# Kernel tuning notes

Hardware: AMD Instinct MI355X
Metric: run time of the kernel (lower is better)

## Reference

```python
import jax, jax.numpy as jnp
import numpy as np

B, N = 8, 2048
IN_F, MID1, HID, MID2, OUT_F = 128, 128, 128, 128, 128
BIG = 9e15  # matches torch's 9000000000000000.0 additive mask constant


def _linear_params(key, out_d, in_d):
    # torch Linear layout: W is [out, in]
    kw, kb = jax.random.split(key)
    w = jax.random.normal(kw, (out_d, in_d), jnp.float32) * (1.0 / np.sqrt(in_d))
    b = jax.random.normal(kb, (out_d,), jnp.float32) * 0.01
    return w, b


def setup_inputs() -> dict:
    key = jax.random.key(0)
    ks = jax.random.split(key, 16)
    h = jax.random.normal(ks[0], (B, N, IN_F), jnp.float32)
    adj = jax.random.randint(ks[1], (B, N, N), 0, 2).astype(jnp.float32)
    vae2_fetures = jax.random.normal(ks[2], (B, N, OUT_F), jnp.float32)
    Wv1, bv1 = _linear_params(ks[3], MID1, IN_F)
    Wk1, bk1 = _linear_params(ks[4], MID1, IN_F)
    Wq1, bq1 = _linear_params(ks[5], MID1, IN_F)
    Wo1, bo1 = _linear_params(ks[6], HID, MID1)
    Wv2, bv2 = _linear_params(ks[7], MID2, HID)
    Wk2, bk2 = _linear_params(ks[8], MID2, HID)
    Wq2, bq2 = _linear_params(ks[9], MID2, HID)
    Wo2, bo2 = _linear_params(ks[10], OUT_F, MID2)
    Wf, bf = _linear_params(ks[11], OUT_F, 2 * OUT_F)
    return {
        "h": h, "adj": adj, "vae2_fetures": vae2_fetures,
        "Wv1": Wv1, "bv1": bv1, "Wk1": Wk1, "bk1": bk1, "Wq1": Wq1, "bq1": bq1,
        "Wo1": Wo1, "bo1": bo1,
        "Wv2": Wv2, "bv2": bv2, "Wk2": Wk2, "bk2": bk2, "Wq2": Wq2, "bq2": bq2,
        "Wo2": Wo2, "bo2": bo2, "Wf": Wf, "bf": bf,
    }


def _lin(x, W, b):
    return jnp.einsum('bnd,od->bno', x, W) + b


def _masked_att_block(x, adj, Wq, bq, Wk, bk, Wv, bv):
    v = jax.nn.relu(_lin(x, Wv, bv))          # [B,N,D]
    q = jax.nn.relu(_lin(x, Wq, bq))          # [B,N,D]
    k = jax.nn.relu(_lin(x, Wk, bk))          # [B,N,D]
    s = jnp.einsum('bnd,bmd->bnm', q, k)       # [B,N,N]
    masked = s * adj - BIG * (1.0 - adj)       # multiplicative + additive mask
    att = jax.nn.softmax(masked, axis=-1)
    return jnp.einsum('bnm,bmd->bnd', att, v)


def reference(h, adj, vae2_fetures,
              Wv1, bv1, Wk1, bk1, Wq1, bq1, Wo1, bo1,
              Wv2, bv2, Wk2, bk2, Wq2, bq2, Wo2, bo2,
              Wf, bf):
    f1 = _masked_att_block(h, adj, Wq1, bq1, Wk1, bk1, Wv1, bv1)
    f1 = _lin(f1, Wo1, bo1)                    # [B,N,HID]
    f2 = _masked_att_block(f1, adj, Wq2, bq2, Wk2, bk2, Wv2, bv2)
    f2 = _lin(f2, Wo2, bo2)                    # [B,N,OUT_F]
    f3 = jnp.concatenate([f2, vae2_fetures], axis=2)
    return _lin(f3, Wf, bf)                    # [B,N,OUT_F]
```

## Files before the change

kernel.cpp:

```cpp
#include <hip/hip_runtime.h>

typedef short s16x8 __attribute__((ext_vector_type(8)));
typedef float f32x4 __attribute__((ext_vector_type(4)));
typedef unsigned short u16x4v __attribute__((ext_vector_type(4)));

#define NSPLIT 4
#define NROWS 16384
#define MSHIFT 44.0f

__device__ __forceinline__ unsigned short f2bf(float f) {
  union { float fl; unsigned int i; } v; v.fl = f;
  unsigned int x = v.i;
  x += 0x7fffu + ((x >> 16) & 1u);
  return (unsigned short)(x >> 16);
}
__device__ __forceinline__ s16x8 load8_bf16(const unsigned short* p) {
  return *(const s16x8*)p;
}
__device__ __forceinline__ s16x8 load8_f32(const float* p) {
  float4 a = *(const float4*)p;
  float4 b = *(const float4*)(p + 4);
  s16x8 r;
  r[0] = (short)f2bf(a.x); r[1] = (short)f2bf(a.y);
  r[2] = (short)f2bf(a.z); r[3] = (short)f2bf(a.w);
  r[4] = (short)f2bf(b.x); r[5] = (short)f2bf(b.y);
  r[6] = (short)f2bf(b.z); r[7] = (short)f2bf(b.w);
  return r;
}
__device__ __forceinline__ int vperm(int nn) {
  return (nn & ~31) | (((nn >> 2) & 3) << 3) | (((nn >> 4) & 1) << 2);
}

__device__ __forceinline__ void gload16(const void* g, void* l) {
  __builtin_amdgcn_global_load_lds(
      (const __attribute__((address_space(1))) void*)g,
      (__attribute__((address_space(3))) void*)l, 16, 0, 0);
}

__device__ __forceinline__ void pack_adj_body(
    const float* __restrict__ ADJ, unsigned long long* __restrict__ MASK,
    int pblk)
{
  const int t = threadIdx.x;
  const int w = t >> 6;
  const int lane = t & 63;
  const int row0 = pblk * 32 + w * 8;

  for (int i = 0; i < 8; ++i) {
    const int row = row0 + i;
    const float4* src = (const float4*)(ADJ + (size_t)row * 2048);
    float4 v[8];
#pragma unroll
    for (int j = 0; j < 8; ++j) v[j] = src[j * 64 + lane];

    unsigned long long wm = 0ull;
#pragma unroll
    for (int j = 0; j < 8; ++j) {
      const unsigned long long b0 = __ballot(v[j].x != 0.f);
      wm = (lane == j * 4 + 0) ? b0 : wm;
      const unsigned long long b1 = __ballot(v[j].y != 0.f);
      wm = (lane == j * 4 + 1) ? b1 : wm;
      const unsigned long long b2 = __ballot(v[j].z != 0.f);
      wm = (lane == j * 4 + 2) ? b2 : wm;
      const unsigned long long b3 = __ballot(v[j].w != 0.f);
      wm = (lane == j * 4 + 3) ? b3 : wm;
    }
    if (lane < 32) MASK[(size_t)row * 32 + lane] = wm;
  }
}

__device__ __forceinline__ void qkv_merged_body(
    const float* __restrict__ X,
    const float* __restrict__ Wq, const float* __restrict__ bq, unsigned short* __restrict__ oq,
    const float* __restrict__ Wk, const float* __restrict__ bk, unsigned short* __restrict__ ok,
    const float* __restrict__ Wv, const float* __restrict__ bv, unsigned short* __restrict__ ovt)
{
  const int t = threadIdx.x;
  const int w = t >> 6;
  const int lane = t & 63;
  const int l15 = lane & 15;
  const int quad = lane >> 4;
  const int mbase = blockIdx.x * 64;

  s16x8 af[4][4];
#pragma unroll
  for (int mt = 0; mt < 4; ++mt) {
    const float* ar = X + (size_t)(mbase + mt * 16 + l15) * 128;
#pragma unroll
    for (int ks = 0; ks < 4; ++ks) af[mt][ks] = load8_f32(ar + ks * 32 + quad * 8);
  }

  const float* Ws[3] = {Wq, Wk, Wv};
  const float* bs[3] = {bq, bk, bv};
  unsigned short* outs[3] = {oq, ok, ovt};

#pragma unroll
  for (int which = 0; which < 3; ++which) {
    const float* W = Ws[which];
    const float* bias = bs[which];
    unsigned short* out = outs[which];
#pragma unroll
    for (int nt = 0; nt < 2; ++nt) {
      const int n = (w * 2 + nt) * 16 + l15;
      const float* wr = W + (size_t)n * 128;
      s16x8 wf[4];
#pragma unroll
      for (int ks = 0; ks < 4; ++ks) wf[ks] = load8_f32(wr + ks * 32 + quad * 8);
      f32x4 acc[4];
#pragma unroll
      for (int mt = 0; mt < 4; ++mt) acc[mt] = (f32x4){0.f, 0.f, 0.f, 0.f};
#pragma unroll
      for (int mt = 0; mt < 4; ++mt)
#pragma unroll
        for (int ks = 0; ks < 4; ++ks)
          acc[mt] = __builtin_amdgcn_mfma_f32_16x16x32_bf16(af[mt][ks], wf[ks], acc[mt], 0, 0, 0);
      const float bv_ = bias[n];
      if (which < 2) {
#pragma unroll
        for (int mt = 0; mt < 4; ++mt)
#pragma unroll
          for (int r = 0; r < 4; ++r)
            out[(size_t)(mbase + mt * 16 + quad * 4 + r) * 128 + n] =
                f2bf(fmaxf(acc[mt][r] + bv_, 0.f));
      } else {
        const int b = mbase >> 11;
#pragma unroll
        for (int mt = 0; mt < 4; ++mt) {
          const int nn = (mbase & 2047) + mt * 16 + quad * 4;
          u16x4v pk;
#pragma unroll
          for (int r = 0; r < 4; ++r) pk[r] = f2bf(fmaxf(acc[mt][r] + bv_, 0.f));
          *(u16x4v*)(out + (size_t)(b * 128 + n) * 2048 + vperm(nn)) = pk;
        }
      }
    }
  }
}

__global__ __launch_bounds__(256) void qkv1_kernel(
    const float* __restrict__ x,
    const float* __restrict__ Wq, const float* __restrict__ bq, unsigned short* __restrict__ oq,
    const float* __restrict__ Wk, const float* __restrict__ bk, unsigned short* __restrict__ ok,
    const float* __restrict__ Wv, const float* __restrict__ bv, unsigned short* __restrict__ ovt,
    const float* __restrict__ adj, unsigned long long* __restrict__ mask)
{
  if (blockIdx.x < 256) qkv_merged_body(x, Wq, bq, oq, Wk, bk, ok, Wv, bv, ovt);
  else                  pack_adj_body(adj, mask, blockIdx.x - 256);
}

__global__ __launch_bounds__(256, 2) void attn_kernel(
    const unsigned short* __restrict__ Q,
    const unsigned short* __restrict__ K,
    const unsigned short* __restrict__ VT,
    const unsigned long long* __restrict__ MASK,
    float* __restrict__ pO, float* __restrict__ pl)
{
  __shared__ __align__(16) unsigned short kbuf[2][64][128];
  __shared__ __align__(16) unsigned short vbuf[2][128][64];

  const int t = threadIdx.x;
  const int w = t >> 6;
  const int lane = t & 63;
  const int l15 = lane & 15;
  const int quad = lane >> 4;
  const int x7 = l15 & 7;

  const int gq0 = blockIdx.x * 128;
  const int b   = gq0 >> 11;
  const int wq0 = (gq0 & 2047) + w * 32;
  const int kc0 = blockIdx.y * (2048 / NSPLIT);

  const unsigned short* Kb  = K  + (size_t)(b * 2048) * 128;
  const unsigned short* VTb = VT + (size_t)(b * 128) * 2048;
  const unsigned long long* Mb = MASK + (size_t)b * 2048 * 32;

  const int krow = t >> 4;
  const int kc16 = t & 15;
  const int kchunk = kc16 ^ (krow & 7);
  const int vrow = t >> 3;
  const int vc16 = t & 7;
  const int vchunk = vc16 ^ (vrow & 7);

  s16x8 qf[2][4];
#pragma unroll
  for (int mt = 0; mt < 2; ++mt) {
    const unsigned short* qrow = Q + (size_t)(gq0 + w * 32 + mt * 16 + l15) * 128;
#pragma unroll
    for (int ks = 0; ks < 4; ++ks) qf[mt][ks] = load8_bf16(qrow + ks * 32 + quad * 8);
  }

  s16x8 ones;
#pragma unroll
  for (int i = 0; i < 8; ++i) ones[i] = (short)0x3F80;

  f32x4 accO[2][8];
  f32x4 accL[2];
#pragma unroll
  for (int mt = 0; mt < 2; ++mt) {
    accL[mt] = (f32x4){0.f, 0.f, 0.f, 0.f};
#pragma unroll
    for (int dt = 0; dt < 8; ++dt) accO[mt][dt] = (f32x4){0.f, 0.f, 0.f, 0.f};
  }

#pragma unroll
  for (int i = 0; i < 4; ++i)
    gload16(Kb + (size_t)(kc0 + i * 16 + krow) * 128 + kchunk * 8,
            &kbuf[0][i * 16 + krow][kc16 * 8]);
#pragma unroll
  for (int i = 0; i < 4; ++i)
    gload16(VTb + (size_t)(i * 32 + vrow) * 2048 + kc0 + vchunk * 8,
            &vbuf[0][i * 32 + vrow][vc16 * 8]);

  __syncthreads();

  for (int g = 0; g < 2; ++g) {
    const int jj = (kc0 >> 8) + g;
    ulonglong2 m01[2], m23[2];
#pragma unroll
    for (int mt = 0; mt < 2; ++mt) {
      const unsigned long long* mrow = Mb + (size_t)(wq0 + mt * 16 + l15) * 32 + jj * 4;
      m01[mt] = *(const ulonglong2*)mrow;
      m23[mt] = *(const ulonglong2*)(mrow + 2);
    }

#pragma unroll
    for (int cg = 0; cg < 4; ++cg) {
      const int kc = kc0 + g * 256 + cg * 64;
      unsigned short (*kb)[128] = kbuf[cg & 1];
      unsigned short (*vb)[64]  = vbuf[cg & 1];

      if (g == 0 || cg < 3) {
        unsigned short (*kbn)[128] = kbuf[(cg + 1) & 1];
        unsigned short (*vbn)[64]  = vbuf[(cg + 1) & 1];
#pragma unroll
        for (int i = 0; i < 4; ++i)
          gload16(Kb + (size_t)(kc + 64 + i * 16 + krow) * 128 + kchunk * 8,
                  &kbn[i * 16 + krow][kc16 * 8]);
#pragma unroll
        for (int i = 0; i < 4; ++i)
          gload16(VTb + (size_t)(i * 32 + vrow) * 2048 + (kc + 64) + vchunk * 8,
                  &vbn[i * 32 + vrow][vc16 * 8]);
      }

      f32x4 sv[2][4];
#pragma unroll
      for (int nt = 0; nt < 4; ++nt) {
        sv[0][nt] = (f32x4){0.f, 0.f, 0.f, 0.f};
        sv[1][nt] = (f32x4){0.f, 0.f, 0.f, 0.f};
      }
      __builtin_amdgcn_s_setprio(1);
#pragma unroll
      for (int nt = 0; nt < 4; ++nt)
#pragma unroll
        for (int ks = 0; ks < 4; ++ks) {
          s16x8 kf = *(const s16x8*)&kb[nt * 16 + l15][((ks * 4 + quad) ^ x7) * 8];
          sv[0][nt] = __builtin_amdgcn_mfma_f32_16x16x32_bf16(kf, qf[0][ks], sv[0][nt], 0, 0, 0);
          sv[1][nt] = __builtin_amdgcn_mfma_f32_16x16x32_bf16(kf, qf[1][ks], sv[1][nt], 0, 0, 0);
        }
      __builtin_amdgcn_s_setprio(0);

      s16x8 pf[2][2];
#pragma unroll
      for (int mt = 0; mt < 2; ++mt) {
        const unsigned long long bse0 = m01[mt].x >> (cg * 16 + quad);
        const unsigned long long bse1 = m01[mt].y >> (cg * 16 + quad);
        const unsigned long long bse2 = m23[mt].x >> (cg * 16 + quad);
        const unsigned long long bse3 = m23[mt].y >> (cg * 16 + quad);
#pragma unroll
        for (int ks = 0; ks < 2; ++ks) {
          s16x8 v;
#pragma unroll
          for (int half = 0; half < 2; ++half) {
            const int nt = ks * 2 + half;
#pragma unroll
            for (int r = 0; r < 4; ++r) {
              const float e = __expf(sv[mt][nt][r] - MSHIFT);
              const unsigned long long bw = (r == 0) ? bse0 : (r == 1) ? bse1
                                          : (r == 2) ? bse2 : bse3;
              const bool keep = (bw >> (nt * 4)) & 1ull;
              v[half * 4 + r] = (short)f2bf(keep ? e : 0.f);
            }
          }
          pf[mt][ks] = v;
        }
      }

      __builtin_amdgcn_s_setprio(1);
#pragma unroll
      for (int mt = 0; mt < 2; ++mt)
#pragma unroll
        for (int ks = 0; ks < 2; ++ks)
          accL[mt] = __builtin_amdgcn_mfma_f32_16x16x32_bf16(ones, pf[mt][ks], accL[mt], 0, 0, 0);

#pragma unroll
      for (int dt = 0; dt < 8; ++dt)
#pragma unroll
        for (int ks = 0; ks < 2; ++ks) {
          s16x8 vf = *(const s16x8*)&vb[dt * 16 + l15][((ks * 4 + quad) ^ x7) * 8];
          accO[0][dt] = __builtin_amdgcn_mfma_f32_16x16x32_bf16(vf, pf[0][ks], accO[0][dt], 0, 0, 0);
          accO[1][dt] = __builtin_amdgcn_mfma_f32_16x16x32_bf16(vf, pf[1][ks], accO[1][dt], 0, 0, 0);
        }
      __builtin_amdgcn_s_setprio(0);

      __syncthreads();
    }
  }

  float* pOs = pO + (size_t)blockIdx.y * NROWS * 128;
#pragma unroll
  for (int mt = 0; mt < 2; ++mt) {
    const int qg = gq0 + w * 32 + mt * 16 + l15;
#pragma unroll
    for (int dt = 0; dt < 8; ++dt)
      *(f32x4*)(pOs + (size_t)qg * 128 + dt * 16 + quad * 4) = accO[mt][dt];
  }
  if (quad == 0) {
#pragma unroll
    for (int mt = 0; mt < 2; ++mt)
      pl[blockIdx.y * NROWS + gq0 + w * 32 + mt * 16 + l15] = accL[mt][0];
  }
}

__device__ __forceinline__ void combine64(
    const float* __restrict__ pO, const float* __restrict__ pl, int grow0,
    unsigned short (*At)[136])
{
  const int t = threadIdx.x;
#pragma unroll
  for (int u = 0; u < 4; ++u) {
    const int unit = u * 256 + t;
    const int row = unit >> 4;
    const int col8 = (unit & 15) * 8;
    const int grow = grow0 + row;
    float lsum = 0.f;
#pragma unroll
    for (int s = 0; s < NSPLIT; ++s) lsum += pl[s * NROWS + grow];
    const float inv = (lsum > 0.f) ? 1.f / lsum : 0.f;
    float acc8[8];
#pragma unroll
    for (int i = 0; i < 8; ++i) acc8[i] = 0.f;
#pragma unroll
    for (int s = 0; s < NSPLIT; ++s) {
      const float* p = pO + (size_t)s * NROWS * 128 + (size_t)grow * 128 + col8;
      float4 x0 = *(const float4*)p;
      float4 x1 = *(const float4*)(p + 4);
      acc8[0] += x0.x; acc8[1] += x0.y; acc8[2] += x0.z; acc8[3] += x0.w;
      acc8[4] += x1.x; acc8[5] += x1.y; acc8[6] += x1.z; acc8[7] += x1.w;
    }
#pragma unroll
    for (int i = 0; i < 8; ++i) At[row][col8 + i] = f2bf(acc8[i] * inv);
  }
}

__global__ __launch_bounds__(256) void redqkv_kernel(
    const float* __restrict__ pO, const float* __restrict__ pl,
    const float* __restrict__ Wo, const float* __restrict__ bo,
    const float* __restrict__ Wq, const float* __restrict__ bq, unsigned short* __restrict__ oq,
    const float* __restrict__ Wk, const float* __restrict__ bk, unsigned short* __restrict__ ok,
    const float* __restrict__ Wv, const float* __restrict__ bv, unsigned short* __restrict__ ovt)
{
  __shared__ __align__(16) unsigned short At[64][136];
  __shared__ __align__(16) unsigned short Bt[64][136];
  const int t = threadIdx.x;
  const int grow0 = blockIdx.x * 64;

  combine64(pO, pl, grow0, At);
  __syncthreads();

  const int w = t >> 6;
  const int lane = t & 63;
  const int l15 = lane & 15;
  const int quad = lane >> 4;

  s16x8 af[4][4];
#pragma unroll
  for (int mt = 0; mt < 4; ++mt)
#pragma unroll
    for (int ks = 0; ks < 4; ++ks)
      af[mt][ks] = *(const s16x8*)&At[mt * 16 + l15][ks * 32 + quad * 8];

#pragma unroll
  for (int nt = 0; nt < 2; ++nt) {
    const int n = (w * 2 + nt) * 16 + l15;
    const float* wr = Wo + (size_t)n * 128;
    s16x8 wf[4];
#pragma unroll
    for (int ks = 0; ks < 4; ++ks) wf[ks] = load8_f32(wr + ks * 32 + quad * 8);
    f32x4 acc[4];
#pragma unroll
    for (int mt = 0; mt < 4; ++mt) acc[mt] = (f32x4){0.f, 0.f, 0.f, 0.f};
#pragma unroll
    for (int mt = 0; mt < 4; ++mt)
#pragma unroll
      for (int ks = 0; ks < 4; ++ks)
        acc[mt] = __builtin_amdgcn_mfma_f32_16x16x32_bf16(af[mt][ks], wf[ks], acc[mt], 0, 0, 0);
    const float bv_ = bo[n];
#pragma unroll
    for (int mt = 0; mt < 4; ++mt)
#pragma unroll
      for (int r = 0; r < 4; ++r)
        Bt[mt * 16 + quad * 4 + r][n] = f2bf(acc[mt][r] + bv_);
  }
  __syncthreads();

  s16x8 a2[4][4];
#pragma unroll
  for (int mt = 0; mt < 4; ++mt)
#pragma unroll
    for (int ks = 0; ks < 4; ++ks)
      a2[mt][ks] = *(const s16x8*)&Bt[mt * 16 + l15][ks * 32 + quad * 8];

#pragma unroll
  for (int which = 0; which < 3; ++which) {
    const float* W = (which == 0) ? Wq : (which == 1) ? Wk : Wv;
    const float* bb = (which == 0) ? bq : (which == 1) ? bk : bv;
    unsigned short* out = (which == 0) ? oq : (which == 1) ? ok : ovt;
#pragma unroll
    for (int nt = 0; nt < 2; ++nt) {
      const int n = (w * 2 + nt) * 16 + l15;
      const float* wr = W + (size_t)n * 128;
      s16x8 wf[4];
#pragma unroll
      for (int ks = 0; ks < 4; ++ks) wf[ks] = load8_f32(wr + ks * 32 + quad * 8);
      f32x4 acc[4];
#pragma unroll
      for (int mt = 0; mt < 4; ++mt) acc[mt] = (f32x4){0.f, 0.f, 0.f, 0.f};
#pragma unroll
      for (int mt = 0; mt < 4; ++mt)
#pragma unroll
        for (int ks = 0; ks < 4; ++ks)
          acc[mt] = __builtin_amdgcn_mfma_f32_16x16x32_bf16(a2[mt][ks], wf[ks], acc[mt], 0, 0, 0);
      const float bv_ = bb[n];
      if (which < 2) {
#pragma unroll
        for (int mt = 0; mt < 4; ++mt)
#pragma unroll
          for (int r = 0; r < 4; ++r)
            out[(size_t)(grow0 + mt * 16 + quad * 4 + r) * 128 + n] =
                f2bf(fmaxf(acc[mt][r] + bv_, 0.f));
      } else {
        const int b = grow0 >> 11;
#pragma unroll
        for (int mt = 0; mt < 4; ++mt) {
          const int nn = (grow0 & 2047) + mt * 16 + quad * 4;
          u16x4v pk;
#pragma unroll
          for (int r = 0; r < 4; ++r) pk[r] = f2bf(fmaxf(acc[mt][r] + bv_, 0.f));
          *(u16x4v*)(out + (size_t)(b * 128 + n) * 2048 + vperm(nn)) = pk;
        }
      }
    }
  }
}

__global__ __launch_bounds__(256) void redfinal_kernel(
    const float* __restrict__ pO, const float* __restrict__ pl,
    const float* __restrict__ Wo, const float* __restrict__ bo,
    const float* __restrict__ Wf, const float* __restrict__ bff,
    const float* __restrict__ vae2, float* __restrict__ out)
{
  __shared__ __align__(16) unsigned short At[64][136];
  __shared__ __align__(16) unsigned short Bt[64][136];
  const int t = threadIdx.x;
  const int grow0 = blockIdx.x * 64;

  combine64(pO, pl, grow0, At);
  __syncthreads();

  const int w = t >> 6;
  const int lane = t & 63;
  const int l15 = lane & 15;
  const int quad = lane >> 4;

  s16x8 af[4][4];
#pragma unroll
  for (int mt = 0; mt < 4; ++mt)
#pragma unroll
    for (int ks = 0; ks < 4; ++ks)
      af[mt][ks] = *(const s16x8*)&At[mt * 16 + l15][ks * 32 + quad * 8];

#pragma unroll
  for (int nt = 0; nt < 2; ++nt) {
    const int n = (w * 2 + nt) * 16 + l15;
    const float* wr = Wo + (size_t)n * 128;
    s16x8 wf[4];
#pragma unroll
    for (int ks = 0; ks < 4; ++ks) wf[ks] = load8_f32(wr + ks * 32 + quad * 8);
    f32x4 acc[4];
#pragma unroll
    for (int mt = 0; mt < 4; ++mt) acc[mt] = (f32x4){0.f, 0.f, 0.f, 0.f};
#pragma unroll
    for (int mt = 0; mt < 4; ++mt)
#pragma unroll
      for (int ks = 0; ks < 4; ++ks)
        acc[mt] = __builtin_amdgcn_mfma_f32_16x16x32_bf16(af[mt][ks], wf[ks], acc[mt], 0, 0, 0);
    const float bv_ = bo[n];
#pragma unroll
    for (int mt = 0; mt < 4; ++mt)
#pragma unroll
      for (int r = 0; r < 4; ++r)
        Bt[mt * 16 + quad * 4 + r][n] = f2bf(acc[mt][r] + bv_);
  }
  __syncthreads();

  s16x8 a1[4][4], a2[4][4];
#pragma unroll
  for (int mt = 0; mt < 4; ++mt) {
#pragma unroll
    for (int ks = 0; ks < 4; ++ks)
      a1[mt][ks] = *(const s16x8*)&Bt[mt * 16 + l15][ks * 32 + quad * 8];
    const float* vrow = vae2 + (size_t)(grow0 + mt * 16 + l15) * 128;
#pragma unroll
    for (int ks = 0; ks < 4; ++ks) a2[mt][ks] = load8_f32(vrow + ks * 32 + quad * 8);
  }

#pragma unroll
  for (int nt = 0; nt < 2; ++nt) {
    const int n = (w * 2 + nt) * 16 + l15;
    const float* wr = Wf + (size_t)n * 256;
    s16x8 wfl[4], wfr[4];
#pragma unroll
    for (int ks = 0; ks < 4; ++ks) {
      wfl[ks] = load8_f32(wr + ks * 32 + quad * 8);
      wfr[ks] = load8_f32(wr + 128 + ks * 32 + quad * 8);
    }
    f32x4 acc[4];
#pragma unroll
    for (int mt = 0; mt < 4; ++mt) acc[mt] = (f32x4){0.f, 0.f, 0.f, 0.f};
#pragma unroll
    for (int mt = 0; mt < 4; ++mt) {
#pragma unroll
      for (int ks = 0; ks < 4; ++ks)
        acc[mt] = __builtin_amdgcn_mfma_f32_16x16x32_bf16(a1[mt][ks], wfl[ks], acc[mt], 0, 0, 0);
#pragma unroll
      for (int ks = 0; ks < 4; ++ks)
        acc[mt] = __builtin_amdgcn_mfma_f32_16x16x32_bf16(a2[mt][ks], wfr[ks], acc[mt], 0, 0, 0);
    }
    const float bv_ = bff[n];
#pragma unroll
    for (int mt = 0; mt < 4; ++mt)
#pragma unroll
      for (int r = 0; r < 4; ++r)
        out[(size_t)(grow0 + mt * 16 + quad * 4 + r) * 128 + n] = acc[mt][r] + bv_;
  }
}

extern "C" void kernel_launch(void* const* d_in, const int* in_sizes, int n_in,
                              void* d_out, int out_size, void* d_ws, size_t ws_size,
                              hipStream_t stream)
{
  const float* h    = (const float*)d_in[0];
  const float* adj  = (const float*)d_in[1];
  const float* vae2 = (const float*)d_in[2];
  const float* Wv1  = (const float*)d_in[3];
  const float* bv1  = (const float*)d_in[4];
  const float* Wk1  = (const float*)d_in[5];
  const float* bk1  = (const float*)d_in[6];
  const float* Wq1  = (const float*)d_in[7];
  const float* bq1  = (const float*)d_in[8];
  const float* Wo1  = (const float*)d_in[9];
  const float* bo1  = (const float*)d_in[10];
  const float* Wv2  = (const float*)d_in[11];
  const float* bv2  = (const float*)d_in[12];
  const float* Wk2  = (const float*)d_in[13];
  const float* bk2  = (const float*)d_in[14];
  const float* Wq2  = (const float*)d_in[15];
  const float* bq2  = (const float*)d_in[16];
  const float* Wo2  = (const float*)d_in[17];
  const float* bo2  = (const float*)d_in[18];
  const float* Wf   = (const float*)d_in[19];
  const float* bff  = (const float*)d_in[20];

  char* wsb = (char*)d_ws;
  const size_t MB = 1u << 20;
  unsigned short* s_q  = (unsigned short*)(wsb + 0 * MB);
  unsigned short* s_k  = (unsigned short*)(wsb + 4 * MB);
  unsigned short* s_vt = (unsigned short*)(wsb + 8 * MB);
  unsigned long long* maskp = (unsigned long long*)(wsb + 12 * MB);
  float* pO = (float*)(wsb + 16 * MB);
  float* pl = (float*)(wsb + 48 * MB);

  qkv1_kernel<<<dim3(256 + 512), dim3(256), 0, stream>>>(
      h, Wq1, bq1, s_q, Wk1, bk1, s_k, Wv1, bv1, s_vt, adj, maskp);
  attn_kernel<<<dim3(128, NSPLIT), dim3(256), 0, stream>>>(
      s_q, s_k, s_vt, maskp, pO, pl);
  redqkv_kernel<<<dim3(256), dim3(256), 0, stream>>>(
      pO, pl, Wo1, bo1, Wq2, bq2, s_q, Wk2, bk2, s_k, Wv2, bv2, s_vt);
  attn_kernel<<<dim3(128, NSPLIT), dim3(256), 0, stream>>>(
      s_q, s_k, s_vt, maskp, pO, pl);
  redfinal_kernel<<<dim3(256), dim3(256), 0, stream>>>(
      pO, pl, Wo2, bo2, Wf, bff, vae2, (float*)d_out);
}
```

Measured before the change: 357.2 us.

## Repack adjacency mask per-lane without ballots and split pack into separate kernel

Adjacency packing now has each lane read 32 contiguous floats and build a 32-bit word directly, instead of using 32 wavefront ballots per row. The bit layout is arranged so the attention kernel can take each lane's keep bits from one 32-bit word with simple shifts, rather than from four shifted 64-bit words. The fused qkv+pack launch is split into two separate kernels, which adds one launch and removes the concurrency between the GEMM and the pack. Per-lane contiguous 128-byte loads may coalesce less well than the previous strided float4 pattern.

```diff
diff --git a/kernel.cpp b/kernel.cpp
--- a/kernel.cpp
+++ b/kernel.cpp
@@ -37,39 +37,34 @@
       (__attribute__((address_space(3))) void*)l, 16, 0, 0);
 }
 
-__device__ __forceinline__ void pack_adj_body(
-    const float* __restrict__ ADJ, unsigned long long* __restrict__ MASK,
-    int pblk)
+__global__ __launch_bounds__(256) void pack_kernel(
+    const float* __restrict__ ADJ, unsigned int* __restrict__ MASK32)
 {
   const int t = threadIdx.x;
   const int w = t >> 6;
   const int lane = t & 63;
-  const int row0 = pblk * 32 + w * 8;
+  const int row0 = blockIdx.x * 32 + w * 8;
 
   for (int i = 0; i < 8; ++i) {
     const int row = row0 + i;
-    const float4* src = (const float4*)(ADJ + (size_t)row * 2048);
+    const float4* src = (const float4*)(ADJ + (size_t)row * 2048 + lane * 32);
     float4 v[8];
 #pragma unroll
-    for (int j = 0; j < 8; ++j) v[j] = src[j * 64 + lane];
-
-    unsigned long long wm = 0ull;
+    for (int j = 0; j < 8; ++j) v[j] = src[j];
+
+    unsigned int wm = 0u;
 #pragma unroll
     for (int j = 0; j < 8; ++j) {
-      const unsigned long long b0 = __ballot(v[j].x != 0.f);
-      wm = (lane == j * 4 + 0) ? b0 : wm;
-      const unsigned long long b1 = __ballot(v[j].y != 0.f);
-      wm = (lane == j * 4 + 1) ? b1 : wm;
-      const unsigned long long b2 = __ballot(v[j].z != 0.f);
-      wm = (lane == j * 4 + 2) ? b2 : wm;
-      const unsigned long long b3 = __ballot(v[j].w != 0.f);
-      wm = (lane == j * 4 + 3) ? b3 : wm;
-    }
-    if (lane < 32) MASK[(size_t)row * 32 + lane] = wm;
-  }
-}
-
-__device__ __forceinline__ void qkv_merged_body(
+      wm |= (v[j].x != 0.f ? 1u : 0u) << (4 * j);
+      wm |= (v[j].y != 0.f ? 2u : 0u) << (4 * j);
+      wm |= (v[j].z != 0.f ? 4u : 0u) << (4 * j);
+      wm |= (v[j].w != 0.f ? 8u : 0u) << (4 * j);
+    }
+    MASK32[(size_t)row * 64 + lane] = wm;
+  }
+}
+
+__global__ __launch_bounds__(256) void gemm_kernel(
     const float* __restrict__ X,
     const float* __restrict__ Wq, const float* __restrict__ bq, unsigned short* __restrict__ oq,
     const float* __restrict__ Wk, const float* __restrict__ bk, unsigned short* __restrict__ ok,
@@ -137,22 +132,11 @@
   }
 }
 
-__global__ __launch_bounds__(256) void qkv1_kernel(
-    const float* __restrict__ x,
-    const float* __restrict__ Wq, const float* __restrict__ bq, unsigned short* __restrict__ oq,
-    const float* __restrict__ Wk, const float* __restrict__ bk, unsigned short* __restrict__ ok,
-    const float* __restrict__ Wv, const float* __restrict__ bv, unsigned short* __restrict__ ovt,
-    const float* __restrict__ adj, unsigned long long* __restrict__ mask)
-{
-  if (blockIdx.x < 256) qkv_merged_body(x, Wq, bq, oq, Wk, bk, ok, Wv, bv, ovt);
-  else                  pack_adj_body(adj, mask, blockIdx.x - 256);
-}
-
 __global__ __launch_bounds__(256, 2) void attn_kernel(
     const unsigned short* __restrict__ Q,
     const unsigned short* __restrict__ K,
     const unsigned short* __restrict__ VT,
-    const unsigned long long* __restrict__ MASK,
+    const unsigned int* __restrict__ MASK32,
     float* __restrict__ pO, float* __restrict__ pl)
 {
   __shared__ __align__(16) unsigned short kbuf[2][64][128];
@@ -172,7 +156,7 @@
 
   const unsigned short* Kb  = K  + (size_t)(b * 2048) * 128;
   const unsigned short* VTb = VT + (size_t)(b * 128) * 2048;
-  const unsigned long long* Mb = MASK + (size_t)b * 2048 * 32;
+  const unsigned int* Mb32 = MASK32 + (size_t)b * 2048 * 64;
 
   const int krow = t >> 4;
   const int kc16 = t & 15;
@@ -215,12 +199,13 @@
 
   for (int g = 0; g < 2; ++g) {
     const int jj = (kc0 >> 8) + g;
-    ulonglong2 m01[2], m23[2];
+    uint4 ua[2], ub[2];
 #pragma unroll
     for (int mt = 0; mt < 2; ++mt) {
-      const unsigned long long* mrow = Mb + (size_t)(wq0 + mt * 16 + l15) * 32 + jj * 4;
-      m01[mt] = *(const ulonglong2*)mrow;
-      m23[mt] = *(const ulonglong2*)(mrow + 2);
+      const unsigned int* mrow =
+          Mb32 + (size_t)(wq0 + mt * 16 + l15) * 64 + jj * 8;
+      ua[mt] = *(const uint4*)mrow;
+      ub[mt] = *(const uint4*)(mrow + 4);
     }
 
 #pragma unroll
@@ -262,12 +247,15 @@
       s16x8 pf[2][2];
 #pragma unroll
       for (int mt = 0; mt < 2; ++mt) {
-        const unsigned long long bse0 = m01[mt].x >> (cg * 16 + quad);
-        const unsigned long long bse1 = m01[mt].y >> (cg * 16 + quad);
-        const unsigned long long bse2 = m23[mt].x >> (cg * 16 + quad);
-        const unsigned long long bse3 = m23[mt].y >> (cg * 16 + quad);
+        const unsigned int wA = (cg == 0) ? ua[mt].x : (cg == 1) ? ua[mt].z
+                               : (cg == 2) ? ub[mt].x : ub[mt].z;
+        const unsigned int wB = (cg == 0) ? ua[mt].y : (cg == 1) ? ua[mt].w
+                               : (cg == 2) ? ub[mt].y : ub[mt].w;
+        const unsigned int bA = wA >> (quad * 4);
+        const unsigned int bB = wB >> (quad * 4);
 #pragma unroll
         for (int ks = 0; ks < 2; ++ks) {
+          const unsigned int bits = (ks == 0) ? bA : bB;
           s16x8 v;
 #pragma unroll
           for (int half = 0; half < 2; ++half) {
@@ -275,9 +263,7 @@
 #pragma unroll
             for (int r = 0; r < 4; ++r) {
               const float e = __expf(sv[mt][nt][r] - MSHIFT);
-              const unsigned long long bw = (r == 0) ? bse0 : (r == 1) ? bse1
-                                          : (r == 2) ? bse2 : bse3;
-              const bool keep = (bw >> (nt * 4)) & 1ull;
+              const bool keep = (bits >> (half * 16 + r)) & 1u;
               v[half * 4 + r] = (short)f2bf(keep ? e : 0.f);
             }
           }
@@ -576,12 +562,13 @@
   unsigned short* s_q  = (unsigned short*)(wsb + 0 * MB);
   unsigned short* s_k  = (unsigned short*)(wsb + 4 * MB);
   unsigned short* s_vt = (unsigned short*)(wsb + 8 * MB);
-  unsigned long long* maskp = (unsigned long long*)(wsb + 12 * MB);
+  unsigned int* maskp  = (unsigned int*)(wsb + 12 * MB);
   float* pO = (float*)(wsb + 16 * MB);
   float* pl = (float*)(wsb + 48 * MB);
 
-  qkv1_kernel<<<dim3(256 + 512), dim3(256), 0, stream>>>(
-      h, Wq1, bq1, s_q, Wk1, bk1, s_k, Wv1, bv1, s_vt, adj, maskp);
+  gemm_kernel<<<dim3(256), dim3(256), 0, stream>>>(
+      h, Wq1, bq1, s_q, Wk1, bk1, s_k, Wv1, bv1, s_vt);
+  pack_kernel<<<dim3(512), dim3(256), 0, stream>>>(adj, maskp);
   attn_kernel<<<dim3(128, NSPLIT), dim3(256), 0, stream>>>(
       s_q, s_k, s_vt, maskp, pO, pl);
   redqkv_kernel<<<dim3(256), dim3(256), 0, stream>>>(
```

Result: faster. 343.6 us, median of 2 (-3.8%).
